# Kernel tuning notes

Measured on AMD Instinct MI355X. Metric: run time of the kernel, lower is better.

The kernel has to match this reference:

```python
import jax, jax.numpy as jnp
import numpy as np

C = 256; GC = 32; G = C // GC; K = 3; S = 1; NEW = 2; PAD = (K - 1) // 2
IN1 = C * K * 2 + C * K * K // 32          # 1608
OUT1 = G * NEW * NEW * K * K // 4          # 72
OUT2 = G * NEW * NEW * K * K               # 288
B = 8; H = 56; W = 56


def setup_inputs():
    key = jax.random.key(0)
    k0, k1, k2 = jax.random.split(key, 3)
    inputs = jax.random.normal(k0, (B, C, H, W), jnp.float32)
    W1 = jax.random.normal(k1, (OUT1, IN1), jnp.float32) * np.float32(1.0 / np.sqrt(IN1))
    b1 = jnp.zeros((OUT1,), jnp.float32)
    W2 = jax.random.normal(k2, (OUT2, OUT1), jnp.float32) * np.float32(1.0 / np.sqrt(OUT1))
    b2 = jnp.zeros((OUT2,), jnp.float32)
    return {"inputs": inputs, "W1": W1, "b1": b1, "W2": W2, "b2": b2}


def _unfold(x, h, w):
    # torch.nn.Unfold(K, 1, PAD, S): patches of shape (B, C, K, K, h, w)
    xp = jnp.pad(x, ((0, 0), (0, 0), (PAD, PAD), (PAD, PAD)))
    cols = [xp[:, :, di:di + (h - 1) * S + 1:S, dj:dj + (w - 1) * S + 1:S]
            for di in range(K) for dj in range(K)]  # fixed K*K=9 slices
    return jnp.stack(cols, axis=2).reshape(x.shape[0], x.shape[1], K, K, h, w)


def reference(inputs, W1, b1, W2, b2):
    b, c, Hh, Ww = inputs.shape
    h = (Hh + 2 * PAD - K) // S + 1
    w = (Ww + 2 * PAD - K) // S + 1
    # (B, G, GC, K, K, h, w)
    x = _unfold(inputs, h, w).reshape(b, G, GC, K, K, h, w)
    # three max-pooled descriptors over different axes
    x1 = x.reshape(b, G, -1, GC // 32, K, K, h, w).max(axis=2).reshape(b, -1, h, w)  # (B, C*K*K//32, h, w)
    x2 = x.max(axis=3).reshape(b, -1, h, w)  # (B, C*K, h, w)
    x3 = x.max(axis=4).reshape(b, -1, h, w)  # (B, C*K, h, w)
    feat = jnp.concatenate([x1, x2, x3], axis=1)  # (B, IN1, h, w)
    # two biased 1x1 convs (ConvModule with no norm/act)
    y = jnp.einsum('bchw,oc->bohw', feat, W1) + b1[None, :, None, None]
    y = jnp.einsum('bchw,oc->bohw', y, W2) + b2[None, :, None, None]
    # softmax over the K*K kernel-window dim
    wgt = jax.nn.softmax(y.reshape(b, G, K * K, NEW * NEW, h, w), axis=2)
    # softmax-weighted local aggregation: sum over kernel window
    agg = jnp.einsum('bgckhw,bgknhw->bgcnhw', x.reshape(b, G, GC, K * K, h, w), wgt)
    # fold with non-overlapping (NEW, NEW) blocks == block upsampling reshape
    return agg.reshape(b, C, NEW, NEW, h, w).transpose(0, 1, 4, 2, 5, 3).reshape(b, C, h * NEW, w * NEW)
```

## Files before the change

kernel.cpp:

```cpp
#include <hip/hip_runtime.h>

#define CC   256
#define HH   56
#define WWID 56
#define KIN1 1608
#define KP1  1632
#define NO1  72
#define NO2  288
#define PPB  14
#define H2   112
#define W2D  112

typedef unsigned short u16;
typedef unsigned int   u32;
typedef __attribute__((ext_vector_type(8))) short v8s;
typedef __attribute__((ext_vector_type(4))) float v4f;

#define W1BF_ELEMS (80 * KP1)
#define W2BF_OFF_B 262144

#define LDS_TOTAL 32768
#define OFF_A 0
#define OFF_B 21504
#define OFF_C 29696

#define Y2S 300

#define SWZ(row) (((row) & 7) << 3)

__device__ __forceinline__ u16 f2b(float x) {
  u32 u = __float_as_uint(x);
  u = (u + 0x7FFFu + ((u >> 16) & 1u)) >> 16;
  return (u16)u;
}

#define DPPMAX(m, ctrl)                                                          \
  do {                                                                           \
    int _y = __builtin_amdgcn_update_dpp(0, __float_as_int(m), (ctrl), 0xF, 0xF, false); \
    (m) = fmaxf((m), __int_as_float(_y));                                        \
  } while (0)

__global__ void kConvW(const float* __restrict__ W1, const float* __restrict__ W2,
                       u16* __restrict__ w1bf, u16* __restrict__ w2bf) {
  int idx = blockIdx.x * 256 + threadIdx.x;
  if (idx < W1BF_ELEMS) {
    int m = idx / KP1, k = idx - m * KP1;
    float v = 0.f;
    if (m < NO1) {
      int orig = -1;
      if (k < 768)                 orig = 72 + (k & 255) * 3 + (k >> 8);
      else if (k < 1536)           orig = 840 + (k & 255) * 3 + ((k - 768) >> 8);
      else if ((k - 1536) < NO1)   orig = k - 1536;
      if (orig >= 0) v = W1[m * KIN1 + orig];
    }
    w1bf[idx] = f2b(v);
  } else {
    int i2 = idx - W1BF_ELEMS;
    if (i2 < NO2 * 96) {
      int m = i2 / 96, k = i2 - m * 96;
      w2bf[i2] = (k < NO1) ? f2b(W2[m * NO1 + k]) : (u16)0;
    }
  }
}

__global__ __launch_bounds__(256, 4)
void kFused(const float* __restrict__ in, const u16* __restrict__ w1bf,
            const float* __restrict__ b1, const u16* __restrict__ w2bf,
            const float* __restrict__ b2, float* __restrict__ out) {
  __shared__ __align__(16) char lds[LDS_TOTAL];
  u16*   rowmaxT = (u16*)(lds + OFF_A);
  u16*   colmaxT = (u16*)(lds + OFF_B);
  u16*   x1T     = (u16*)(lds + OFF_C);
  float* partA   = (float*)(lds + OFF_A);
  float* y2L     = (float*)(lds + OFF_A);
  float* tile    = (float*)(lds + OFF_A);

  const int t  = threadIdx.x;
  const int L  = blockIdx.x + 4 * (blockIdx.y + 56 * blockIdx.z);
  const int jq = L >> 3;
  const int jt = jq & 3, i = jq >> 2, b = L & 7;
  const int c  = t;
  const int g  = c >> 5;
  const int gc = c & 31;
  const int w  = t >> 6, lane = t & 63;
  const int ml = lane & 15, quad = lane >> 4;

  {
    u32* xu = (u32*)x1T;
    if (t < 132) {
#pragma unroll
      for (int rp2 = 0; rp2 < 2; ++rp2) {
        int idx = 2 * t + rp2;
        if (idx < 192) {
          int row = idx / 12;
          xu[(row * 48 + 36 + (idx - row * 12)) ^ ((row & 7) << 2)] = 0u;
        } else {
          int e = idx - 192, row = 14 + e / 36;
          xu[(row * 48 + (e % 36)) ^ ((row & 7) << 2)] = 0u;
        }
      }
    }
  }

  const float* rowbase0 = in + ((size_t)b * CC + c) * (HH * WWID);
  u32 win_p[3][8];
  float colmax[16];
#pragma unroll
  for (int k = 0; k < 16; ++k) colmax[k] = -3.0e38f;

#pragma unroll
  for (int r = 0; r < 3; ++r) {
    const int row = i - 1 + r;
    float sc[16];
    if (row < 0 || row >= HH) {
#pragma unroll
      for (int k = 0; k < 16; ++k) sc[k] = 0.f;
    } else {
      const float* rp = rowbase0 + row * WWID;
      float l[20];
      if (jt == 0) {
        const float4 a0 = *(const float4*)(rp), a1 = *(const float4*)(rp + 4),
                     a2 = *(const float4*)(rp + 8), a3 = *(const float4*)(rp + 12);
        l[0]=a0.x;l[1]=a0.y;l[2]=a0.z;l[3]=a0.w; l[4]=a1.x;l[5]=a1.y;l[6]=a1.z;l[7]=a1.w;
        l[8]=a2.x;l[9]=a2.y;l[10]=a2.z;l[11]=a2.w; l[12]=a3.x;l[13]=a3.y;l[14]=a3.z;l[15]=a3.w;
        sc[0] = 0.f;
#pragma unroll
        for (int k = 1; k < 16; ++k) sc[k] = l[k - 1];
      } else if (jt == 3) {
        const float* q = rp + 40;
        const float4 a0 = *(const float4*)(q), a1 = *(const float4*)(q + 4),
                     a2 = *(const float4*)(q + 8), a3 = *(const float4*)(q + 12);
        l[0]=a0.x;l[1]=a0.y;l[2]=a0.z;l[3]=a0.w; l[4]=a1.x;l[5]=a1.y;l[6]=a1.z;l[7]=a1.w;
        l[8]=a2.x;l[9]=a2.y;l[10]=a2.z;l[11]=a2.w; l[12]=a3.x;l[13]=a3.y;l[14]=a3.z;l[15]=a3.w;
#pragma unroll
        for (int k = 0; k < 15; ++k) sc[k] = l[k + 1];
        sc[15] = 0.f;
      } else {
        const float* q = rp + ((jt == 1) ? 12 : 24);
        const float4 a0 = *(const float4*)(q), a1 = *(const float4*)(q + 4),
                     a2 = *(const float4*)(q + 8), a3 = *(const float4*)(q + 12),
                     a4 = *(const float4*)(q + 16);
        l[0]=a0.x;l[1]=a0.y;l[2]=a0.z;l[3]=a0.w; l[4]=a1.x;l[5]=a1.y;l[6]=a1.z;l[7]=a1.w;
        l[8]=a2.x;l[9]=a2.y;l[10]=a2.z;l[11]=a2.w; l[12]=a3.x;l[13]=a3.y;l[14]=a3.z;l[15]=a3.w;
        l[16]=a4.x;l[17]=a4.y;l[18]=a4.z;l[19]=a4.w;
        if (jt == 1) {
#pragma unroll
          for (int k = 0; k < 16; ++k) sc[k] = l[k + 1];
        } else {
#pragma unroll
          for (int k = 0; k < 16; ++k) sc[k] = l[k + 3];
        }
      }
    }
#pragma unroll
    for (int k = 0; k < 16; ++k) colmax[k] = fmaxf(colmax[k], sc[k]);
#pragma unroll
    for (int n = 0; n < 14; ++n)
      rowmaxT[(n * 768 + r * 256 + c) ^ SWZ(n)] =
          f2b(fmaxf(fmaxf(sc[n], sc[n + 1]), sc[n + 2]));
#pragma unroll
    for (int col = 0; col < 16; ++col) {
      float m = sc[col];
      DPPMAX(m, 0xB1);
      DPPMAX(m, 0x4E);
      DPPMAX(m, 0x141);
      DPPMAX(m, 0x140);
      { int y = __builtin_amdgcn_ds_swizzle(__float_as_int(m), 0x401F);
        m = fmaxf(m, __int_as_float(y)); }
      if (gc == col) {
        u16 mv = f2b(m);
#pragma unroll
        for (int kj = 0; kj < 3; ++kj) {
          const int n = col - kj;
          if (n >= 0 && n < 14)
            x1T[(n * 96 + g * 9 + r * 3 + kj) ^ SWZ(n)] = mv;
        }
      }
    }
#pragma unroll
    for (int k = 0; k < 8; ++k)
      win_p[r][k] = (u32)f2b(sc[2 * k]) | ((u32)f2b(sc[2 * k + 1]) << 16);
  }
#pragma unroll
  for (int col = 0; col < 16; ++col)
    colmaxT[(col * 256 + c) ^ SWZ(col)] = f2b(colmax[col]);
  __syncthreads();

  v4f acc[5];
#pragma unroll
  for (int mt = 0; mt < 5; ++mt) acc[mt] = (v4f){0.f, 0.f, 0.f, 0.f};
  const int ks0 = w * 13, ks1 = (w == 3) ? 51 : ks0 + 13;

  auto loadB = [&](int ks) -> v8s {
    if (ks < 24) {
      int kj = ks >> 3, c0 = (ks & 7) * 32, rowi = ml + kj;
      return *(v8s*)&colmaxT[(rowi * 256 + c0 + quad * 8) ^ SWZ(rowi)];
    } else if (ks < 48) {
      return *(v8s*)&rowmaxT[(ml * 768 + (ks - 24) * 32 + quad * 8) ^ SWZ(ml)];
    } else {
      return *(v8s*)&x1T[(ml * 96 + (ks - 48) * 32 + quad * 8) ^ SWZ(ml)];
    }
  };

  {
    v8s bf_c = loadB(ks0);
    v8s af_c[5];
    {
      const int k0 = ks0 * 32 + quad * 8;
#pragma unroll
      for (int mt = 0; mt < 5; ++mt)
        af_c[mt] = *(const v8s*)&w1bf[(mt * 16 + ml) * KP1 + k0];
    }
    for (int ks = ks0; ks < ks1; ++ks) {
      v8s bf_n, af_n[5];
      if (ks + 1 < ks1) {
        bf_n = loadB(ks + 1);
        const int k0n = (ks + 1) * 32 + quad * 8;
#pragma unroll
        for (int mt = 0; mt < 5; ++mt)
          af_n[mt] = *(const v8s*)&w1bf[(mt * 16 + ml) * KP1 + k0n];
      }
#pragma unroll
      for (int mt = 0; mt < 5; ++mt)
        acc[mt] = __builtin_amdgcn_mfma_f32_16x16x32_bf16(af_c[mt], bf_c, acc[mt], 0, 0, 0);
      if (ks + 1 < ks1) {
        bf_c = bf_n;
#pragma unroll
        for (int mt = 0; mt < 5; ++mt) af_c[mt] = af_n[mt];
      }
    }
  }
  __syncthreads();

#pragma unroll
  for (int mt = 0; mt < 5; ++mt)
    *(v4f*)&partA[((w * 5 + mt) * 16 + ml) * 16 + quad * 4] = acc[mt];
  __syncthreads();

  u16* y1b = x1T;
#pragma unroll
  for (int it = 0; it < 4; ++it) {
    int e = t + it * 256;
    if (e < NO1 * PPB) {
      int m = e / PPB, n = e - m * PPB;
      float s = b1[m];
#pragma unroll
      for (int ww = 0; ww < 4; ++ww)
        s += partA[((ww * 5 + (m >> 4)) * 16 + n) * 16 + (m & 15)];
      y1b[(n * 96 + m) ^ SWZ(n)] = f2b(s);
    }
  }
  __syncthreads();

  {
    v8s bfr[3];
#pragma unroll
    for (int ks = 0; ks < 3; ++ks)
      bfr[ks] = *(v8s*)&y1b[(ml * 96 + ks * 32 + quad * 8) ^ SWZ(ml)];
    const int mt0 = (w < 2) ? 5 * w : 10 + 4 * (w - 2);
    const int mtn = (w < 2) ? 5 : 4;
    const u16* w2base = w2bf + ml * 96 + quad * 8;
    v8s afA[3], afB[3];
#pragma unroll
    for (int ks = 0; ks < 3; ++ks)
      afA[ks] = *(const v8s*)(w2base + (mt0 * 16) * 96 + ks * 32);
#pragma unroll
    for (int mi = 0; mi < 5; ++mi) {
      if (mi < mtn) {
        const int mt = mt0 + mi;
        v4f a2 = (v4f){0.f, 0.f, 0.f, 0.f};
        if ((mi & 1) == 0) {
          if (mi + 1 < mtn) {
#pragma unroll
            for (int ks = 0; ks < 3; ++ks)
              afB[ks] = *(const v8s*)(w2base + ((mt + 1) * 16) * 96 + ks * 32);
          }
#pragma unroll
          for (int ks = 0; ks < 3; ++ks)
            a2 = __builtin_amdgcn_mfma_f32_16x16x32_bf16(afA[ks], bfr[ks], a2, 0, 0, 0);
        } else {
          if (mi + 1 < mtn) {
#pragma unroll
            for (int ks = 0; ks < 3; ++ks)
              afA[ks] = *(const v8s*)(w2base + ((mt + 1) * 16) * 96 + ks * 32);
          }
#pragma unroll
          for (int ks = 0; ks < 3; ++ks)
            a2 = __builtin_amdgcn_mfma_f32_16x16x32_bf16(afB[ks], bfr[ks], a2, 0, 0, 0);
        }
        const int o0 = mt * 16 + quad * 4;
        const float4 bv = *(const float4*)(b2 + o0);
        a2[0] += bv.x; a2[1] += bv.y; a2[2] += bv.z; a2[3] += bv.w;
        *(v4f*)&y2L[ml * Y2S + o0] = a2;
      }
    }
  }
  __syncthreads();

#pragma unroll
  for (int it = 0; it < 2; ++it) {
    int s2 = t + it * 256;
    if (s2 < 448) {
      int gg = s2 / 56, rem = s2 - gg * 56, nn = rem / PPB, n = rem - nn * PPB;
      float* bp = &y2L[n * Y2S + gg * 36 + nn];
      float v9[9], m = -1e30f;
#pragma unroll
      for (int k = 0; k < 9; ++k) { v9[k] = bp[k * 4]; m = fmaxf(m, v9[k]); }
      float sum = 0.f;
#pragma unroll
      for (int k = 0; k < 9; ++k) { v9[k] = __expf(v9[k] - m); sum += v9[k]; }
      float inv = 1.f / sum;
#pragma unroll
      for (int k = 0; k < 9; ++k) bp[k * 4] = v9[k] * inv;
    }
  }
  __syncthreads();

  float a0s[14], a1s[14], a2s[14], a3s[14];
#pragma unroll
  for (int n = 0; n < 14; ++n) {
    const v4f* wp = (const v4f*)&y2L[n * Y2S + g * 36];
    float a0 = 0.f, a1 = 0.f, a2v = 0.f, a3 = 0.f;
#pragma unroll
    for (int r = 0; r < 3; ++r) {
      float x0, x1, x2v;
      if ((n & 1) == 0) {
        u32 ua = win_p[r][n >> 1], ub = win_p[r][(n >> 1) + 1];
        x0  = __uint_as_float(ua << 16);
        x1  = __uint_as_float(ua & 0xffff0000u);
        x2v = __uint_as_float(ub << 16);
      } else {
        u32 ua = win_p[r][n >> 1], ub = win_p[r][(n >> 1) + 1];
        x0  = __uint_as_float(ua & 0xffff0000u);
        x1  = __uint_as_float(ub << 16);
        x2v = __uint_as_float(ub & 0xffff0000u);
      }
#pragma unroll
      for (int kj = 0; kj < 3; ++kj) {
        v4f wv = wp[r * 3 + kj];
        float x = (kj == 0) ? x0 : (kj == 1) ? x1 : x2v;
        a0  = fmaf(x, wv[0], a0);
        a1  = fmaf(x, wv[1], a1);
        a2v = fmaf(x, wv[2], a2v);
        a3  = fmaf(x, wv[3], a3);
      }
    }
    a0s[n] = a0; a1s[n] = a1; a2s[n] = a2v; a3s[n] = a3;
  }
  __syncthreads();

  const int cl = c & 63;
  for (int ch = 0; ch < 4; ++ch) {
    if ((c >> 6) == ch) {
#pragma unroll
      for (int n = 0; n < 14; ++n) {
        float2 lo2; lo2.x = a0s[n]; lo2.y = a1s[n];
        float2 hi2; hi2.x = a2s[n]; hi2.y = a3s[n];
        *(float2*)&tile[cl * 60 + 2 * n] = lo2;
        *(float2*)&tile[cl * 60 + 28 + 2 * n] = hi2;
      }
    }
    __syncthreads();
#pragma unroll
    for (int it = 0; it < 4; ++it) {
      int f = t + it * 256;
      if (f < 896) {
        int rr = f / 7, xi = f - rr * 7;
        int cg = ch * 64 + (rr >> 1), di = rr & 1;
        v4f val = *(v4f*)&tile[(rr >> 1) * 60 + di * 28 + xi * 4];
        *(v4f*)&out[((size_t)(b * CC + cg) * H2 + (size_t)(2 * i + di)) * W2D
                    + 28 * jt + xi * 4] = val;
      }
    }
    __syncthreads();
  }
}

extern "C" void kernel_launch(void* const* d_in, const int* in_sizes, int n_in,
                              void* d_out, int out_size, void* d_ws, size_t ws_size,
                              hipStream_t stream) {
  const float* in = (const float*)d_in[0];
  const float* W1 = (const float*)d_in[1];
  const float* b1 = (const float*)d_in[2];
  const float* W2 = (const float*)d_in[3];
  const float* b2 = (const float*)d_in[4];
  float* out = (float*)d_out;

  u16* w1bf = (u16*)d_ws;
  u16* w2bf = (u16*)((char*)d_ws + W2BF_OFF_B);

  const int B = in_sizes[0] / (CC * HH * WWID);

  kConvW<<<dim3((W1BF_ELEMS + NO2 * 96 + 255) / 256), 256, 0, stream>>>(W1, W2, w1bf, w2bf);
  dim3 grid(WWID / PPB, HH, B);
  kFused<<<grid, 256, 0, stream>>>(in, w1bf, b1, w2bf, b2, out);
}
```

Before: 201.2 us.

## Prefetch GEMM weights before barriers and double-buffer the MFMA loop with priority hints

```diff
diff --git a/kernel.cpp b/kernel.cpp
--- a/kernel.cpp
+++ b/kernel.cpp
@@ -42,23 +42,35 @@
 
 __global__ void kConvW(const float* __restrict__ W1, const float* __restrict__ W2,
                        u16* __restrict__ w1bf, u16* __restrict__ w2bf) {
-  int idx = blockIdx.x * 256 + threadIdx.x;
-  if (idx < W1BF_ELEMS) {
-    int m = idx / KP1, k = idx - m * KP1;
-    float v = 0.f;
+  int p = blockIdx.x * 256 + threadIdx.x;
+  int e0 = 2 * p;
+  float v0 = 0.f, v1 = 0.f;
+  if (e0 < W1BF_ELEMS) {
+    int m = e0 / KP1, k = e0 - m * KP1;
     if (m < NO1) {
-      int orig = -1;
-      if (k < 768)                 orig = 72 + (k & 255) * 3 + (k >> 8);
-      else if (k < 1536)           orig = 840 + (k & 255) * 3 + ((k - 768) >> 8);
-      else if ((k - 1536) < NO1)   orig = k - 1536;
-      if (orig >= 0) v = W1[m * KIN1 + orig];
-    }
-    w1bf[idx] = f2b(v);
+      const float* Wm = W1 + m * KIN1;
+      if (k < 768) {
+        int o = 72 + (k & 255) * 3 + (k >> 8);
+        v0 = Wm[o]; v1 = Wm[o + 3];
+      } else if (k < 1536) {
+        int o = 840 + (k & 255) * 3 + ((k - 768) >> 8);
+        v0 = Wm[o]; v1 = Wm[o + 3];
+      } else {
+        int t1 = k - 1536;
+        if (t1 < NO1)     v0 = Wm[t1];
+        if (t1 + 1 < NO1) v1 = Wm[t1 + 1];
+      }
+    }
+    ((u32*)w1bf)[p] = (u32)f2b(v0) | ((u32)f2b(v1) << 16);
   } else {
-    int i2 = idx - W1BF_ELEMS;
+    int i2 = e0 - W1BF_ELEMS;
     if (i2 < NO2 * 96) {
       int m = i2 / 96, k = i2 - m * 96;
-      w2bf[i2] = (k < NO1) ? f2b(W2[m * NO1 + k]) : (u16)0;
+      if (k < NO1) {
+        v0 = W2[m * NO1 + k];
+        if (k + 1 < NO1) v1 = W2[m * NO1 + k + 1];
+      }
+      ((u32*)w2bf)[i2 >> 1] = (u32)f2b(v0) | ((u32)f2b(v1) << 16);
     }
   }
 }
@@ -184,12 +196,15 @@
 #pragma unroll
   for (int col = 0; col < 16; ++col)
     colmaxT[(col * 256 + c) ^ SWZ(col)] = f2b(colmax[col]);
-  __syncthreads();
-
-  v4f acc[5];
-#pragma unroll
-  for (int mt = 0; mt < 5; ++mt) acc[mt] = (v4f){0.f, 0.f, 0.f, 0.f};
+
   const int ks0 = w * 13, ks1 = (w == 3) ? 51 : ks0 + 13;
+  v8s afA[5], afB[5];
+#pragma unroll
+  for (int mt = 0; mt < 5; ++mt) {
+    afA[mt] = *(const v8s*)&w1bf[(mt * 16 + ml) * KP1 + ks0 * 32 + quad * 8];
+    afB[mt] = *(const v8s*)&w1bf[(mt * 16 + ml) * KP1 + (ks0 + 1) * 32 + quad * 8];
+  }
+  __syncthreads();
 
   auto loadB = [&](int ks) -> v8s {
     if (ks < 24) {
@@ -202,31 +217,38 @@
     }
   };
 
+  v4f acc[5];
+#pragma unroll
+  for (int mt = 0; mt < 5; ++mt) acc[mt] = (v4f){0.f, 0.f, 0.f, 0.f};
   {
-    v8s bf_c = loadB(ks0);
-    v8s af_c[5];
-    {
-      const int k0 = ks0 * 32 + quad * 8;
+    v8s bfA = loadB(ks0);
+    v8s bfB = loadB(ks0 + 1);
+    for (int ks = ks0; ks < ks1; ks += 2) {
+      __builtin_amdgcn_s_setprio(1);
 #pragma unroll
       for (int mt = 0; mt < 5; ++mt)
-        af_c[mt] = *(const v8s*)&w1bf[(mt * 16 + ml) * KP1 + k0];
-    }
-    for (int ks = ks0; ks < ks1; ++ks) {
-      v8s bf_n, af_n[5];
+        acc[mt] = __builtin_amdgcn_mfma_f32_16x16x32_bf16(afA[mt], bfA, acc[mt], 0, 0, 0);
+      __builtin_amdgcn_s_setprio(0);
+      if (ks + 2 < ks1) {
+        const int kn = (ks + 2) * 32 + quad * 8;
+#pragma unroll
+        for (int mt = 0; mt < 5; ++mt)
+          afA[mt] = *(const v8s*)&w1bf[(mt * 16 + ml) * KP1 + kn];
+        bfA = loadB(ks + 2);
+      }
       if (ks + 1 < ks1) {
-        bf_n = loadB(ks + 1);
-        const int k0n = (ks + 1) * 32 + quad * 8;
+        __builtin_amdgcn_s_setprio(1);
 #pragma unroll
         for (int mt = 0; mt < 5; ++mt)
-          af_n[mt] = *(const v8s*)&w1bf[(mt * 16 + ml) * KP1 + k0n];
-      }
-#pragma unroll
-      for (int mt = 0; mt < 5; ++mt)
-        acc[mt] = __builtin_amdgcn_mfma_f32_16x16x32_bf16(af_c[mt], bf_c, acc[mt], 0, 0, 0);
-      if (ks + 1 < ks1) {
-        bf_c = bf_n;
-#pragma unroll
-        for (int mt = 0; mt < 5; ++mt) af_c[mt] = af_n[mt];
+          acc[mt] = __builtin_amdgcn_mfma_f32_16x16x32_bf16(afB[mt], bfB, acc[mt], 0, 0, 0);
+        __builtin_amdgcn_s_setprio(0);
+        if (ks + 3 < ks1) {
+          const int kn = (ks + 3) * 32 + quad * 8;
+#pragma unroll
+          for (int mt = 0; mt < 5; ++mt)
+            afB[mt] = *(const v8s*)&w1bf[(mt * 16 + ml) * KP1 + kn];
+          bfB = loadB(ks + 3);
+        }
       }
     }
   }
@@ -235,6 +257,19 @@
 #pragma unroll
   for (int mt = 0; mt < 5; ++mt)
     *(v4f*)&partA[((w * 5 + mt) * 16 + ml) * 16 + quad * 4] = acc[mt];
+
+  const int mt0 = (w < 2) ? 5 * w : 10 + 4 * (w - 2);
+  const int mtn = (w < 2) ? 5 : 4;
+  v8s w2r[15];
+#pragma unroll
+  for (int mi = 0; mi < 5; ++mi) {
+    if (mi < mtn) {
+#pragma unroll
+      for (int ks = 0; ks < 3; ++ks)
+        w2r[mi * 3 + ks] =
+            *(const v8s*)&w2bf[((mt0 + mi) * 16 + ml) * 96 + ks * 32 + quad * 8];
+    }
+  }
   __syncthreads();
 
   u16* y1b = x1T;
@@ -257,41 +292,23 @@
 #pragma unroll
     for (int ks = 0; ks < 3; ++ks)
       bfr[ks] = *(v8s*)&y1b[(ml * 96 + ks * 32 + quad * 8) ^ SWZ(ml)];
-    const int mt0 = (w < 2) ? 5 * w : 10 + 4 * (w - 2);
-    const int mtn = (w < 2) ? 5 : 4;
-    const u16* w2base = w2bf + ml * 96 + quad * 8;
-    v8s afA[3], afB[3];
-#pragma unroll
-    for (int ks = 0; ks < 3; ++ks)
-      afA[ks] = *(const v8s*)(w2base + (mt0 * 16) * 96 + ks * 32);
+    float4 bvA = *(const float4*)(b2 + mt0 * 16 + quad * 4);
 #pragma unroll
     for (int mi = 0; mi < 5; ++mi) {
       if (mi < mtn) {
         const int mt = mt0 + mi;
+        float4 bvB;
+        if (mi + 1 < mtn)
+          bvB = *(const float4*)(b2 + (mt + 1) * 16 + quad * 4);
         v4f a2 = (v4f){0.f, 0.f, 0.f, 0.f};
-        if ((mi & 1) == 0) {
-          if (mi + 1 < mtn) {
-#pragma unroll
-            for (int ks = 0; ks < 3; ++ks)
-              afB[ks] = *(const v8s*)(w2base + ((mt + 1) * 16) * 96 + ks * 32);
-          }
-#pragma unroll
-          for (int ks = 0; ks < 3; ++ks)
-            a2 = __builtin_amdgcn_mfma_f32_16x16x32_bf16(afA[ks], bfr[ks], a2, 0, 0, 0);
-        } else {
-          if (mi + 1 < mtn) {
-#pragma unroll
-            for (int ks = 0; ks < 3; ++ks)
-              afA[ks] = *(const v8s*)(w2base + ((mt + 1) * 16) * 96 + ks * 32);
-          }
-#pragma unroll
-          for (int ks = 0; ks < 3; ++ks)
-            a2 = __builtin_amdgcn_mfma_f32_16x16x32_bf16(afB[ks], bfr[ks], a2, 0, 0, 0);
-        }
-        const int o0 = mt * 16 + quad * 4;
-        const float4 bv = *(const float4*)(b2 + o0);
-        a2[0] += bv.x; a2[1] += bv.y; a2[2] += bv.z; a2[3] += bv.w;
-        *(v4f*)&y2L[ml * Y2S + o0] = a2;
+        __builtin_amdgcn_s_setprio(1);
+#pragma unroll
+        for (int ks = 0; ks < 3; ++ks)
+          a2 = __builtin_amdgcn_mfma_f32_16x16x32_bf16(w2r[mi * 3 + ks], bfr[ks], a2, 0, 0, 0);
+        __builtin_amdgcn_s_setprio(0);
+        a2[0] += bvA.x; a2[1] += bvA.y; a2[2] += bvA.z; a2[3] += bvA.w;
+        *(v4f*)&y2L[ml * Y2S + mt * 16 + quad * 4] = a2;
+        if (mi + 1 < mtn) bvA = bvB;
       }
     }
   }
@@ -391,7 +408,7 @@
 
   const int B = in_sizes[0] / (CC * HH * WWID);
 
-  kConvW<<<dim3((W1BF_ELEMS + NO2 * 96 + 255) / 256), 256, 0, stream>>>(W1, W2, w1bf, w2bf);
+  kConvW<<<dim3(((W1BF_ELEMS + NO2 * 96) / 2 + 255) / 256), 256, 0, stream>>>(W1, W2, w1bf, w2bf);
   dim3 grid(WWID / PPB, HH, B);
   kFused<<<grid, 256, 0, stream>>>(in, w1bf, b1, w2bf, b2, out);
 }
```

After: 225.4 us. 12.0% more time.

## Halve per-block pixel tile to 7 and pack weight conversion two-per-thread

Applied to the files above, without the earlier changes.

```diff
diff --git a/kernel.cpp b/kernel.cpp
--- a/kernel.cpp
+++ b/kernel.cpp
@@ -7,7 +7,7 @@
 #define KP1  1632
 #define NO1  72
 #define NO2  288
-#define PPB  14
+#define PPB  7
 #define H2   112
 #define W2D  112
 
@@ -19,10 +19,10 @@
 #define W1BF_ELEMS (80 * KP1)
 #define W2BF_OFF_B 262144
 
-#define LDS_TOTAL 32768
+#define LDS_TOTAL 16704
 #define OFF_A 0
-#define OFF_B 21504
-#define OFF_C 29696
+#define OFF_B 10752
+#define OFF_C 15360
 
 #define Y2S 300
 
@@ -42,23 +42,35 @@
 
 __global__ void kConvW(const float* __restrict__ W1, const float* __restrict__ W2,
                        u16* __restrict__ w1bf, u16* __restrict__ w2bf) {
-  int idx = blockIdx.x * 256 + threadIdx.x;
-  if (idx < W1BF_ELEMS) {
-    int m = idx / KP1, k = idx - m * KP1;
-    float v = 0.f;
+  int p = blockIdx.x * 256 + threadIdx.x;
+  int e0 = 2 * p;
+  float v0 = 0.f, v1 = 0.f;
+  if (e0 < W1BF_ELEMS) {
+    int m = e0 / KP1, k = e0 - m * KP1;
     if (m < NO1) {
-      int orig = -1;
-      if (k < 768)                 orig = 72 + (k & 255) * 3 + (k >> 8);
-      else if (k < 1536)           orig = 840 + (k & 255) * 3 + ((k - 768) >> 8);
-      else if ((k - 1536) < NO1)   orig = k - 1536;
-      if (orig >= 0) v = W1[m * KIN1 + orig];
-    }
-    w1bf[idx] = f2b(v);
+      const float* Wm = W1 + m * KIN1;
+      if (k < 768) {
+        int o = 72 + (k & 255) * 3 + (k >> 8);
+        v0 = Wm[o]; v1 = Wm[o + 3];
+      } else if (k < 1536) {
+        int o = 840 + (k & 255) * 3 + ((k - 768) >> 8);
+        v0 = Wm[o]; v1 = Wm[o + 3];
+      } else {
+        int t1 = k - 1536;
+        if (t1 < NO1)     v0 = Wm[t1];
+        if (t1 + 1 < NO1) v1 = Wm[t1 + 1];
+      }
+    }
+    ((u32*)w1bf)[p] = (u32)f2b(v0) | ((u32)f2b(v1) << 16);
   } else {
-    int i2 = idx - W1BF_ELEMS;
+    int i2 = e0 - W1BF_ELEMS;
     if (i2 < NO2 * 96) {
       int m = i2 / 96, k = i2 - m * 96;
-      w2bf[i2] = (k < NO1) ? f2b(W2[m * NO1 + k]) : (u16)0;
+      if (k < NO1) {
+        v0 = W2[m * NO1 + k];
+        if (k + 1 < NO1) v1 = W2[m * NO1 + k + 1];
+      }
+      ((u32*)w2bf)[i2 >> 1] = (u32)f2b(v0) | ((u32)f2b(v1) << 16);
     }
   }
 }
@@ -76,90 +88,81 @@
   float* tile    = (float*)(lds + OFF_A);
 
   const int t  = threadIdx.x;
-  const int L  = blockIdx.x + 4 * (blockIdx.y + 56 * blockIdx.z);
+  const int L  = blockIdx.x + 8 * (blockIdx.y + 56 * blockIdx.z);
+  const int b  = L & 7;
   const int jq = L >> 3;
-  const int jt = jq & 3, i = jq >> 2, b = L & 7;
+  const int jt = jq & 7, i = jq >> 3;
   const int c  = t;
   const int g  = c >> 5;
   const int gc = c & 31;
   const int w  = t >> 6, lane = t & 63;
   const int ml = lane & 15, quad = lane >> 4;
+  const int ml_c = (ml < 7) ? ml : 0;
 
   {
     u32* xu = (u32*)x1T;
-    if (t < 132) {
-#pragma unroll
-      for (int rp2 = 0; rp2 < 2; ++rp2) {
-        int idx = 2 * t + rp2;
-        if (idx < 192) {
-          int row = idx / 12;
-          xu[(row * 48 + 36 + (idx - row * 12)) ^ ((row & 7) << 2)] = 0u;
-        } else {
-          int e = idx - 192, row = 14 + e / 36;
-          xu[(row * 48 + (e % 36)) ^ ((row & 7) << 2)] = 0u;
-        }
-      }
+    if (t < 84) {
+      int row = t / 12, j = t - row * 12;
+      xu[(row * 48 + 36 + j) ^ ((row & 7) << 2)] = 0u;
     }
   }
 
   const float* rowbase0 = in + ((size_t)b * CC + c) * (HH * WWID);
-  u32 win_p[3][8];
-  float colmax[16];
-#pragma unroll
-  for (int k = 0; k < 16; ++k) colmax[k] = -3.0e38f;
+  u32 win_p[3][5];
+  float colmax[9];
+#pragma unroll
+  for (int k = 0; k < 9; ++k) colmax[k] = -3.0e38f;
 
 #pragma unroll
   for (int r = 0; r < 3; ++r) {
     const int row = i - 1 + r;
-    float sc[16];
+    float sc[9];
     if (row < 0 || row >= HH) {
 #pragma unroll
-      for (int k = 0; k < 16; ++k) sc[k] = 0.f;
+      for (int k = 0; k < 9; ++k) sc[k] = 0.f;
     } else {
       const float* rp = rowbase0 + row * WWID;
-      float l[20];
       if (jt == 0) {
-        const float4 a0 = *(const float4*)(rp), a1 = *(const float4*)(rp + 4),
-                     a2 = *(const float4*)(rp + 8), a3 = *(const float4*)(rp + 12);
+        const float4 a0 = *(const float4*)(rp), a1 = *(const float4*)(rp + 4);
+        sc[0] = 0.f;
+        sc[1]=a0.x; sc[2]=a0.y; sc[3]=a0.z; sc[4]=a0.w;
+        sc[5]=a1.x; sc[6]=a1.y; sc[7]=a1.z; sc[8]=a1.w;
+      } else if (jt == 7) {
+        const float4 a0 = *(const float4*)(rp + 48), a1 = *(const float4*)(rp + 52);
+        sc[0]=a0.x; sc[1]=a0.y; sc[2]=a0.z; sc[3]=a0.w;
+        sc[4]=a1.x; sc[5]=a1.y; sc[6]=a1.z; sc[7]=a1.w;
+        sc[8] = 0.f;
+      } else {
+        const int f = 7 * jt - 1, off = f & 3;
+        const float* q = rp + (f - off);
+        const float4 a0 = *(const float4*)(q), a1 = *(const float4*)(q + 4),
+                     a2 = *(const float4*)(q + 8);
+        float l[12];
         l[0]=a0.x;l[1]=a0.y;l[2]=a0.z;l[3]=a0.w; l[4]=a1.x;l[5]=a1.y;l[6]=a1.z;l[7]=a1.w;
-        l[8]=a2.x;l[9]=a2.y;l[10]=a2.z;l[11]=a2.w; l[12]=a3.x;l[13]=a3.y;l[14]=a3.z;l[15]=a3.w;
-        sc[0] = 0.f;
-#pragma unroll
-        for (int k = 1; k < 16; ++k) sc[k] = l[k - 1];
-      } else if (jt == 3) {
-        const float* q = rp + 40;
-        const float4 a0 = *(const float4*)(q), a1 = *(const float4*)(q + 4),
-                     a2 = *(const float4*)(q + 8), a3 = *(const float4*)(q + 12);
-        l[0]=a0.x;l[1]=a0.y;l[2]=a0.z;l[3]=a0.w; l[4]=a1.x;l[5]=a1.y;l[6]=a1.z;l[7]=a1.w;
-        l[8]=a2.x;l[9]=a2.y;l[10]=a2.z;l[11]=a2.w; l[12]=a3.x;l[13]=a3.y;l[14]=a3.z;l[15]=a3.w;
-#pragma unroll
-        for (int k = 0; k < 15; ++k) sc[k] = l[k + 1];
-        sc[15] = 0.f;
-      } else {
-        const float* q = rp + ((jt == 1) ? 12 : 24);
-        const float4 a0 = *(const float4*)(q), a1 = *(const float4*)(q + 4),
-                     a2 = *(const float4*)(q + 8), a3 = *(const float4*)(q + 12),
-                     a4 = *(const float4*)(q + 16);
-        l[0]=a0.x;l[1]=a0.y;l[2]=a0.z;l[3]=a0.w; l[4]=a1.x;l[5]=a1.y;l[6]=a1.z;l[7]=a1.w;
-        l[8]=a2.x;l[9]=a2.y;l[10]=a2.z;l[11]=a2.w; l[12]=a3.x;l[13]=a3.y;l[14]=a3.z;l[15]=a3.w;
-        l[16]=a4.x;l[17]=a4.y;l[18]=a4.z;l[19]=a4.w;
-        if (jt == 1) {
-#pragma unroll
-          for (int k = 0; k < 16; ++k) sc[k] = l[k + 1];
+        l[8]=a2.x;l[9]=a2.y;l[10]=a2.z;l[11]=a2.w;
+        if (off == 0) {
+#pragma unroll
+          for (int s = 0; s < 9; ++s) sc[s] = l[s];
+        } else if (off == 1) {
+#pragma unroll
+          for (int s = 0; s < 9; ++s) sc[s] = l[s + 1];
+        } else if (off == 2) {
+#pragma unroll
+          for (int s = 0; s < 9; ++s) sc[s] = l[s + 2];
         } else {
 #pragma unroll
-          for (int k = 0; k < 16; ++k) sc[k] = l[k + 3];
+          for (int s = 0; s < 9; ++s) sc[s] = l[s + 3];
         }
       }
     }
 #pragma unroll
-    for (int k = 0; k < 16; ++k) colmax[k] = fmaxf(colmax[k], sc[k]);
-#pragma unroll
-    for (int n = 0; n < 14; ++n)
+    for (int k = 0; k < 9; ++k) colmax[k] = fmaxf(colmax[k], sc[k]);
+#pragma unroll
+    for (int n = 0; n < 7; ++n)
       rowmaxT[(n * 768 + r * 256 + c) ^ SWZ(n)] =
           f2b(fmaxf(fmaxf(sc[n], sc[n + 1]), sc[n + 2]));
 #pragma unroll
-    for (int col = 0; col < 16; ++col) {
+    for (int col = 0; col < 9; ++col) {
       float m = sc[col];
       DPPMAX(m, 0xB1);
       DPPMAX(m, 0x4E);
@@ -172,17 +175,18 @@
 #pragma unroll
         for (int kj = 0; kj < 3; ++kj) {
           const int n = col - kj;
-          if (n >= 0 && n < 14)
+          if (n >= 0 && n < 7)
             x1T[(n * 96 + g * 9 + r * 3 + kj) ^ SWZ(n)] = mv;
         }
       }
     }
 #pragma unroll
-    for (int k = 0; k < 8; ++k)
+    for (int k = 0; k < 4; ++k)
       win_p[r][k] = (u32)f2b(sc[2 * k]) | ((u32)f2b(sc[2 * k + 1]) << 16);
-  }
-#pragma unroll
-  for (int col = 0; col < 16; ++col)
+    win_p[r][4] = (u32)f2b(sc[8]);
+  }
+#pragma unroll
+  for (int col = 0; col < 9; ++col)
     colmaxT[(col * 256 + c) ^ SWZ(col)] = f2b(colmax[col]);
   __syncthreads();
 
@@ -193,12 +197,12 @@
 
   auto loadB = [&](int ks) -> v8s {
     if (ks < 24) {
-      int kj = ks >> 3, c0 = (ks & 7) * 32, rowi = ml + kj;
+      int kj = ks >> 3, c0 = (ks & 7) * 32, rowi = ml_c + kj;
       return *(v8s*)&colmaxT[(rowi * 256 + c0 + quad * 8) ^ SWZ(rowi)];
     } else if (ks < 48) {
-      return *(v8s*)&rowmaxT[(ml * 768 + (ks - 24) * 32 + quad * 8) ^ SWZ(ml)];
+      return *(v8s*)&rowmaxT[(ml_c * 768 + (ks - 24) * 32 + quad * 8) ^ SWZ(ml_c)];
     } else {
-      return *(v8s*)&x1T[(ml * 96 + (ks - 48) * 32 + quad * 8) ^ SWZ(ml)];
+      return *(v8s*)&x1T[(ml_c * 96 + (ks - 48) * 32 + quad * 8) ^ SWZ(ml_c)];
     }
   };
 
@@ -232,21 +236,23 @@
   }
   __syncthreads();
 
-#pragma unroll
-  for (int mt = 0; mt < 5; ++mt)
-    *(v4f*)&partA[((w * 5 + mt) * 16 + ml) * 16 + quad * 4] = acc[mt];
+  if (ml < 7) {
+#pragma unroll
+    for (int mt = 0; mt < 5; ++mt)
+      *(v4f*)&partA[((w * 5 + mt) * 7 + ml) * 16 + quad * 4] = acc[mt];
+  }
   __syncthreads();
 
   u16* y1b = x1T;
 #pragma unroll
-  for (int it = 0; it < 4; ++it) {
+  for (int it = 0; it < 2; ++it) {
     int e = t + it * 256;
     if (e < NO1 * PPB) {
       int m = e / PPB, n = e - m * PPB;
       float s = b1[m];
 #pragma unroll
       for (int ww = 0; ww < 4; ++ww)
-        s += partA[((ww * 5 + (m >> 4)) * 16 + n) * 16 + (m & 15)];
+        s += partA[((ww * 5 + (m >> 4)) * 7 + n) * 16 + (m & 15)];
       y1b[(n * 96 + m) ^ SWZ(n)] = f2b(s);
     }
   }
@@ -256,7 +262,7 @@
     v8s bfr[3];
 #pragma unroll
     for (int ks = 0; ks < 3; ++ks)
-      bfr[ks] = *(v8s*)&y1b[(ml * 96 + ks * 32 + quad * 8) ^ SWZ(ml)];
+      bfr[ks] = *(v8s*)&y1b[(ml_c * 96 + ks * 32 + quad * 8) ^ SWZ(ml_c)];
     const int mt0 = (w < 2) ? 5 * w : 10 + 4 * (w - 2);
     const int mtn = (w < 2) ? 5 : 4;
     const u16* w2base = w2bf + ml * 96 + quad * 8;
@@ -288,64 +294,63 @@
           for (int ks = 0; ks < 3; ++ks)
             a2 = __builtin_amdgcn_mfma_f32_16x16x32_bf16(afB[ks], bfr[ks], a2, 0, 0, 0);
         }
-        const int o0 = mt * 16 + quad * 4;
-        const float4 bv = *(const float4*)(b2 + o0);
-        a2[0] += bv.x; a2[1] += bv.y; a2[2] += bv.z; a2[3] += bv.w;
-        *(v4f*)&y2L[ml * Y2S + o0] = a2;
-      }
-    }
-  }
-  __syncthreads();
-
-#pragma unroll
-  for (int it = 0; it < 2; ++it) {
-    int s2 = t + it * 256;
-    if (s2 < 448) {
-      int gg = s2 / 56, rem = s2 - gg * 56, nn = rem / PPB, n = rem - nn * PPB;
-      float* bp = &y2L[n * Y2S + gg * 36 + nn];
-      float v9[9], m = -1e30f;
-#pragma unroll
-      for (int k = 0; k < 9; ++k) { v9[k] = bp[k * 4]; m = fmaxf(m, v9[k]); }
-      float sum = 0.f;
-#pragma unroll
-      for (int k = 0; k < 9; ++k) { v9[k] = __expf(v9[k] - m); sum += v9[k]; }
-      float inv = 1.f / sum;
-#pragma unroll
-      for (int k = 0; k < 9; ++k) bp[k * 4] = v9[k] * inv;
-    }
-  }
-  __syncthreads();
-
-  float a0s[14], a1s[14], a2s[14], a3s[14];
-#pragma unroll
-  for (int n = 0; n < 14; ++n) {
-    const v4f* wp = (const v4f*)&y2L[n * Y2S + g * 36];
-    float a0 = 0.f, a1 = 0.f, a2v = 0.f, a3 = 0.f;
+        if (ml < 7) {
+          const int o0 = mt * 16 + quad * 4;
+          const float4 bv = *(const float4*)(b2 + o0);
+          a2[0] += bv.x; a2[1] += bv.y; a2[2] += bv.z; a2[3] += bv.w;
+          *(v4f*)&y2L[ml * Y2S + o0] = a2;
+        }
+      }
+    }
+  }
+  __syncthreads();
+
+  if (t < 224) {
+    int gg = t / 28, rem = t - gg * 28, nn = rem / PPB, n = rem - nn * PPB;
+    float* bp = &y2L[n * Y2S + gg * 36 + nn];
+    float v9[9], m = -1e30f;
+#pragma unroll
+    for (int k = 0; k < 9; ++k) { v9[k] = bp[k * 4]; m = fmaxf(m, v9[k]); }
+    float sum = 0.f;
+#pragma unroll
+    for (int k = 0; k < 9; ++k) { v9[k] = __expf(v9[k] - m); sum += v9[k]; }
+    float inv = 1.f / sum;
+#pragma unroll
+    for (int k = 0; k < 9; ++k) bp[k * 4] = v9[k] * inv;
+  }
+  __syncthreads();
+
+  float a0s[7], a1s[7], a2s[7], a3s[7];
+#pragma unroll
+  for (int x = 0; x < 4; ++x) {
+    const int n0 = 2 * x;
+    const v4f* wp0 = (const v4f*)&y2L[n0 * Y2S + g * 36];
+    const v4f* wp1 = (x < 3) ? (const v4f*)&y2L[(n0 + 1) * Y2S + g * 36] : wp0;
+    float e0 = 0.f, e1 = 0.f, e2 = 0.f, e3 = 0.f;
+    float o0 = 0.f, o1 = 0.f, o2 = 0.f, o3 = 0.f;
 #pragma unroll
     for (int r = 0; r < 3; ++r) {
-      float x0, x1, x2v;
-      if ((n & 1) == 0) {
-        u32 ua = win_p[r][n >> 1], ub = win_p[r][(n >> 1) + 1];
-        x0  = __uint_as_float(ua << 16);
-        x1  = __uint_as_float(ua & 0xffff0000u);
-        x2v = __uint_as_float(ub << 16);
-      } else {
-        u32 ua = win_p[r][n >> 1], ub = win_p[r][(n >> 1) + 1];
-        x0  = __uint_as_float(ua & 0xffff0000u);
-        x1  = __uint_as_float(ub << 16);
-        x2v = __uint_as_float(ub & 0xffff0000u);
-      }
+      u32 ua = win_p[r][x], ub = win_p[r][x + 1];
+      float ex0 = __uint_as_float(ua << 16);
+      float ex1 = __uint_as_float(ua & 0xffff0000u);
+      float ex2 = __uint_as_float(ub << 16);
+      float ox2 = __uint_as_float(ub & 0xffff0000u);
 #pragma unroll
       for (int kj = 0; kj < 3; ++kj) {
-        v4f wv = wp[r * 3 + kj];
-        float x = (kj == 0) ? x0 : (kj == 1) ? x1 : x2v;
-        a0  = fmaf(x, wv[0], a0);
-        a1  = fmaf(x, wv[1], a1);
-        a2v = fmaf(x, wv[2], a2v);
-        a3  = fmaf(x, wv[3], a3);
-      }
-    }
-    a0s[n] = a0; a1s[n] = a1; a2s[n] = a2v; a3s[n] = a3;
+        v4f wv0 = wp0[r * 3 + kj];
+        float xe = (kj == 0) ? ex0 : (kj == 1) ? ex1 : ex2;
+        e0 = fmaf(xe, wv0[0], e0); e1 = fmaf(xe, wv0[1], e1);
+        e2 = fmaf(xe, wv0[2], e2); e3 = fmaf(xe, wv0[3], e3);
+        if (x < 3) {
+          v4f wv1 = wp1[r * 3 + kj];
+          float xo = (kj == 0) ? ex1 : (kj == 1) ? ex2 : ox2;
+          o0 = fmaf(xo, wv1[0], o0); o1 = fmaf(xo, wv1[1], o1);
+          o2 = fmaf(xo, wv1[2], o2); o3 = fmaf(xo, wv1[3], o3);
+        }
+      }
+    }
+    a0s[n0] = e0; a1s[n0] = e1; a2s[n0] = e2; a3s[n0] = e3;
+    if (x < 3) { a0s[n0 + 1] = o0; a1s[n0 + 1] = o1; a2s[n0 + 1] = o2; a3s[n0 + 1] = o3; }
   }
   __syncthreads();
 
@@ -353,11 +358,11 @@
   for (int ch = 0; ch < 4; ++ch) {
     if ((c >> 6) == ch) {
 #pragma unroll
-      for (int n = 0; n < 14; ++n) {
+      for (int n = 0; n < 7; ++n) {
         float2 lo2; lo2.x = a0s[n]; lo2.y = a1s[n];
         float2 hi2; hi2.x = a2s[n]; hi2.y = a3s[n];
-        *(float2*)&tile[cl * 60 + 2 * n] = lo2;
-        *(float2*)&tile[cl * 60 + 28 + 2 * n] = hi2;
+        *(float2*)&tile[cl * 30 + 2 * n] = lo2;
+        *(float2*)&tile[cl * 30 + 14 + 2 * n] = hi2;
       }
     }
     __syncthreads();
@@ -367,9 +372,9 @@
       if (f < 896) {
         int rr = f / 7, xi = f - rr * 7;
         int cg = ch * 64 + (rr >> 1), di = rr & 1;
-        v4f val = *(v4f*)&tile[(rr >> 1) * 60 + di * 28 + xi * 4];
-        *(v4f*)&out[((size_t)(b * CC + cg) * H2 + (size_t)(2 * i + di)) * W2D
-                    + 28 * jt + xi * 4] = val;
+        float2 val = *(float2*)&tile[(rr >> 1) * 30 + di * 14 + xi * 2];
+        *(float2*)&out[((size_t)(b * CC + cg) * H2 + (size_t)(2 * i + di)) * W2D
+                       + 14 * jt + 2 * xi] = val;
       }
     }
     __syncthreads();
@@ -391,7 +396,7 @@
 
   const int B = in_sizes[0] / (CC * HH * WWID);
 
-  kConvW<<<dim3((W1BF_ELEMS + NO2 * 96 + 255) / 256), 256, 0, stream>>>(W1, W2, w1bf, w2bf);
+  kConvW<<<dim3(((W1BF_ELEMS + NO2 * 96) / 2 + 255) / 256), 256, 0, stream>>>(W1, W2, w1bf, w2bf);
   dim3 grid(WWID / PPB, HH, B);
   kFused<<<grid, 256, 0, stream>>>(in, w1bf, b1, w2bf, b2, out);
 }
```

Measured after the change: 229.7 us. 14.2% more time.

## Interleave rowmax GEMM per window row and split W1 GEMM by output tile

Applied to the files above, without the earlier changes.

```diff
diff --git a/kernel.cpp b/kernel.cpp
--- a/kernel.cpp
+++ b/kernel.cpp
@@ -15,14 +15,16 @@
 typedef unsigned int   u32;
 typedef __attribute__((ext_vector_type(8))) short v8s;
 typedef __attribute__((ext_vector_type(4))) float v4f;
+typedef __attribute__((ext_vector_type(4))) unsigned short us4;
 
 #define W1BF_ELEMS (80 * KP1)
 #define W2BF_OFF_B 262144
 
-#define LDS_TOTAL 32768
-#define OFF_A 0
-#define OFF_B 21504
-#define OFF_C 29696
+#define LDS_TOTAL 20736
+#define OFF_CM 0
+#define OFF_RM 8192
+#define OFF_X1 15360
+#define OFF_Y1 18048
 
 #define Y2S 300
 
@@ -42,23 +44,35 @@
 
 __global__ void kConvW(const float* __restrict__ W1, const float* __restrict__ W2,
                        u16* __restrict__ w1bf, u16* __restrict__ w2bf) {
-  int idx = blockIdx.x * 256 + threadIdx.x;
-  if (idx < W1BF_ELEMS) {
-    int m = idx / KP1, k = idx - m * KP1;
-    float v = 0.f;
+  int p = blockIdx.x * 256 + threadIdx.x;
+  int e0 = 2 * p;
+  float v0 = 0.f, v1 = 0.f;
+  if (e0 < W1BF_ELEMS) {
+    int m = e0 / KP1, k = e0 - m * KP1;
     if (m < NO1) {
-      int orig = -1;
-      if (k < 768)                 orig = 72 + (k & 255) * 3 + (k >> 8);
-      else if (k < 1536)           orig = 840 + (k & 255) * 3 + ((k - 768) >> 8);
-      else if ((k - 1536) < NO1)   orig = k - 1536;
-      if (orig >= 0) v = W1[m * KIN1 + orig];
-    }
-    w1bf[idx] = f2b(v);
+      const float* Wm = W1 + m * KIN1;
+      if (k < 768) {
+        int o = 72 + (k & 255) * 3 + (k >> 8);
+        v0 = Wm[o]; v1 = Wm[o + 3];
+      } else if (k < 1536) {
+        int o = 840 + (k & 255) * 3 + ((k - 768) >> 8);
+        v0 = Wm[o]; v1 = Wm[o + 3];
+      } else {
+        int t1 = k - 1536;
+        if (t1 < NO1)     v0 = Wm[t1];
+        if (t1 + 1 < NO1) v1 = Wm[t1 + 1];
+      }
+    }
+    ((u32*)w1bf)[p] = (u32)f2b(v0) | ((u32)f2b(v1) << 16);
   } else {
-    int i2 = idx - W1BF_ELEMS;
+    int i2 = e0 - W1BF_ELEMS;
     if (i2 < NO2 * 96) {
       int m = i2 / 96, k = i2 - m * 96;
-      w2bf[i2] = (k < NO1) ? f2b(W2[m * NO1 + k]) : (u16)0;
+      if (k < NO1) {
+        v0 = W2[m * NO1 + k];
+        if (k + 1 < NO1) v1 = W2[m * NO1 + k + 1];
+      }
+      ((u32*)w2bf)[i2 >> 1] = (u32)f2b(v0) | ((u32)f2b(v1) << 16);
     }
   }
 }
@@ -68,12 +82,13 @@
             const float* __restrict__ b1, const u16* __restrict__ w2bf,
             const float* __restrict__ b2, float* __restrict__ out) {
   __shared__ __align__(16) char lds[LDS_TOTAL];
-  u16*   rowmaxT = (u16*)(lds + OFF_A);
-  u16*   colmaxT = (u16*)(lds + OFF_B);
-  u16*   x1T     = (u16*)(lds + OFF_C);
-  float* partA   = (float*)(lds + OFF_A);
-  float* y2L     = (float*)(lds + OFF_A);
-  float* tile    = (float*)(lds + OFF_A);
+  u16*   colmaxT  = (u16*)(lds + OFF_CM);
+  u16*   rowmax_r = (u16*)(lds + OFF_RM);
+  u16*   x1T      = (u16*)(lds + OFF_X1);
+  u16*   y1b      = (u16*)(lds + OFF_Y1);
+  float* partE    = (float*)(lds + OFF_CM);
+  float* y2L      = (float*)(lds + OFF_CM);
+  float* tile     = (float*)(lds + OFF_CM);
 
   const int t  = threadIdx.x;
   const int L  = blockIdx.x + 4 * (blockIdx.y + 56 * blockIdx.z);
@@ -84,21 +99,16 @@
   const int gc = c & 31;
   const int w  = t >> 6, lane = t & 63;
   const int ml = lane & 15, quad = lane >> 4;
+  const int ml_c = (ml < 14) ? ml : 0;
 
   {
     u32* xu = (u32*)x1T;
-    if (t < 132) {
-#pragma unroll
-      for (int rp2 = 0; rp2 < 2; ++rp2) {
-        int idx = 2 * t + rp2;
-        if (idx < 192) {
-          int row = idx / 12;
-          xu[(row * 48 + 36 + (idx - row * 12)) ^ ((row & 7) << 2)] = 0u;
-        } else {
-          int e = idx - 192, row = 14 + e / 36;
-          xu[(row * 48 + (e % 36)) ^ ((row & 7) << 2)] = 0u;
-        }
-      }
+    u32* yu = (u32*)y1b;
+    if (t < 168) {
+      int row = t / 12, j = t - row * 12;
+      int off = (row * 48 + 36 + j) ^ ((row & 7) << 2);
+      xu[off] = 0u;
+      yu[off] = 0u;
     }
   }
 
@@ -107,6 +117,9 @@
   float colmax[16];
 #pragma unroll
   for (int k = 0; k < 16; ++k) colmax[k] = -3.0e38f;
+
+  v4f acc0 = (v4f){0.f, 0.f, 0.f, 0.f};
+  v4f acc4 = (v4f){0.f, 0.f, 0.f, 0.f};
 
 #pragma unroll
   for (int r = 0; r < 3; ++r) {
@@ -156,7 +169,7 @@
     for (int k = 0; k < 16; ++k) colmax[k] = fmaxf(colmax[k], sc[k]);
 #pragma unroll
     for (int n = 0; n < 14; ++n)
-      rowmaxT[(n * 768 + r * 256 + c) ^ SWZ(n)] =
+      rowmax_r[(n * 256 + c) ^ SWZ(n)] =
           f2b(fmaxf(fmaxf(sc[n], sc[n + 1]), sc[n + 2]));
 #pragma unroll
     for (int col = 0; col < 16; ++col) {
@@ -180,75 +193,78 @@
 #pragma unroll
     for (int k = 0; k < 8; ++k)
       win_p[r][k] = (u32)f2b(sc[2 * k]) | ((u32)f2b(sc[2 * k + 1]) << 16);
-  }
-#pragma unroll
-  for (int col = 0; col < 16; ++col)
-    colmaxT[(col * 256 + c) ^ SWZ(col)] = f2b(colmax[col]);
-  __syncthreads();
-
-  v4f acc[5];
-#pragma unroll
-  for (int mt = 0; mt < 5; ++mt) acc[mt] = (v4f){0.f, 0.f, 0.f, 0.f};
-  const int ks0 = w * 13, ks1 = (w == 3) ? 51 : ks0 + 13;
-
-  auto loadB = [&](int ks) -> v8s {
-    if (ks < 24) {
-      int kj = ks >> 3, c0 = (ks & 7) * 32, rowi = ml + kj;
-      return *(v8s*)&colmaxT[(rowi * 256 + c0 + quad * 8) ^ SWZ(rowi)];
-    } else if (ks < 48) {
-      return *(v8s*)&rowmaxT[(ml * 768 + (ks - 24) * 32 + quad * 8) ^ SWZ(ml)];
-    } else {
-      return *(v8s*)&x1T[(ml * 96 + (ks - 48) * 32 + quad * 8) ^ SWZ(ml)];
-    }
-  };
+    if (r == 2) {
+#pragma unroll
+      for (int col = 0; col < 16; ++col)
+        colmaxT[(col * 256 + c) ^ SWZ(col)] = f2b(colmax[col]);
+    }
+    __syncthreads();
+
+    {
+      const int ksb = 24 + r * 8;
+#pragma unroll
+      for (int ci = 0; ci < 8; ++ci) {
+        v8s bf = *(v8s*)&rowmax_r[(ml_c * 256 + ci * 32 + quad * 8) ^ SWZ(ml_c)];
+        v8s a0 = *(const v8s*)&w1bf[(w * 16 + ml) * KP1 + (ksb + ci) * 32 + quad * 8];
+        acc0 = __builtin_amdgcn_mfma_f32_16x16x32_bf16(a0, bf, acc0, 0, 0, 0);
+      }
+#pragma unroll
+      for (int e = 0; e < 2; ++e) {
+        const int ci = 2 * w + e;
+        v8s bf = *(v8s*)&rowmax_r[(ml_c * 256 + ci * 32 + quad * 8) ^ SWZ(ml_c)];
+        v8s a4 = *(const v8s*)&w1bf[(64 + ml) * KP1 + (ksb + ci) * 32 + quad * 8];
+        acc4 = __builtin_amdgcn_mfma_f32_16x16x32_bf16(a4, bf, acc4, 0, 0, 0);
+      }
+    }
+    if (r < 2) __syncthreads();
+  }
 
   {
-    v8s bf_c = loadB(ks0);
-    v8s af_c[5];
-    {
-      const int k0 = ks0 * 32 + quad * 8;
-#pragma unroll
-      for (int mt = 0; mt < 5; ++mt)
-        af_c[mt] = *(const v8s*)&w1bf[(mt * 16 + ml) * KP1 + k0];
-    }
-    for (int ks = ks0; ks < ks1; ++ks) {
-      v8s bf_n, af_n[5];
-      if (ks + 1 < ks1) {
-        bf_n = loadB(ks + 1);
-        const int k0n = (ks + 1) * 32 + quad * 8;
-#pragma unroll
-        for (int mt = 0; mt < 5; ++mt)
-          af_n[mt] = *(const v8s*)&w1bf[(mt * 16 + ml) * KP1 + k0n];
-      }
-#pragma unroll
-      for (int mt = 0; mt < 5; ++mt)
-        acc[mt] = __builtin_amdgcn_mfma_f32_16x16x32_bf16(af_c[mt], bf_c, acc[mt], 0, 0, 0);
-      if (ks + 1 < ks1) {
-        bf_c = bf_n;
-#pragma unroll
-        for (int mt = 0; mt < 5; ++mt) af_c[mt] = af_n[mt];
-      }
-    }
-  }
-  __syncthreads();
-
-#pragma unroll
-  for (int mt = 0; mt < 5; ++mt)
-    *(v4f*)&partA[((w * 5 + mt) * 16 + ml) * 16 + quad * 4] = acc[mt];
-  __syncthreads();
-
-  u16* y1b = x1T;
-#pragma unroll
-  for (int it = 0; it < 4; ++it) {
-    int e = t + it * 256;
-    if (e < NO1 * PPB) {
-      int m = e / PPB, n = e - m * PPB;
-      float s = b1[m];
-#pragma unroll
-      for (int ww = 0; ww < 4; ++ww)
-        s += partA[((ww * 5 + (m >> 4)) * 16 + n) * 16 + (m & 15)];
-      y1b[(n * 96 + m) ^ SWZ(n)] = f2b(s);
-    }
+#pragma unroll
+    for (int s = 0; s < 24; ++s) {
+      const int kj = s >> 3, ci = s & 7, rowi = ml + kj;
+      v8s bf = *(v8s*)&colmaxT[(rowi * 256 + ci * 32 + quad * 8) ^ SWZ(rowi)];
+      v8s a0 = *(const v8s*)&w1bf[(w * 16 + ml) * KP1 + s * 32 + quad * 8];
+      acc0 = __builtin_amdgcn_mfma_f32_16x16x32_bf16(a0, bf, acc0, 0, 0, 0);
+    }
+#pragma unroll
+    for (int e = 0; e < 6; ++e) {
+      const int s4 = 6 * w + e, kj = s4 >> 3, ci = s4 & 7, rowi = ml + kj;
+      v8s bf = *(v8s*)&colmaxT[(rowi * 256 + ci * 32 + quad * 8) ^ SWZ(rowi)];
+      v8s a4 = *(const v8s*)&w1bf[(64 + ml) * KP1 + s4 * 32 + quad * 8];
+      acc4 = __builtin_amdgcn_mfma_f32_16x16x32_bf16(a4, bf, acc4, 0, 0, 0);
+    }
+#pragma unroll
+    for (int ksx = 0; ksx < 3; ++ksx) {
+      v8s bf = *(v8s*)&x1T[(ml_c * 96 + ksx * 32 + quad * 8) ^ SWZ(ml_c)];
+      v8s a0 = *(const v8s*)&w1bf[(w * 16 + ml) * KP1 + (48 + ksx) * 32 + quad * 8];
+      acc0 = __builtin_amdgcn_mfma_f32_16x16x32_bf16(a0, bf, acc0, 0, 0, 0);
+    }
+    if (w < 3) {
+      v8s bf = *(v8s*)&x1T[(ml_c * 96 + w * 32 + quad * 8) ^ SWZ(ml_c)];
+      v8s a4 = *(const v8s*)&w1bf[(64 + ml) * KP1 + (48 + w) * 32 + quad * 8];
+      acc4 = __builtin_amdgcn_mfma_f32_16x16x32_bf16(a4, bf, acc4, 0, 0, 0);
+    }
+  }
+  __syncthreads();
+
+  *(v4f*)&partE[((w * 16 + ml) * 16) + quad * 4] = acc4;
+  if (ml < 14) {
+    const float4 bv0 = *(const float4*)(b1 + w * 16 + quad * 4);
+    us4 h0;
+    h0.x = f2b(acc0[0] + bv0.x); h0.y = f2b(acc0[1] + bv0.y);
+    h0.z = f2b(acc0[2] + bv0.z); h0.w = f2b(acc0[3] + bv0.w);
+    *(us4*)&y1b[(ml * 96 + w * 16 + quad * 4) ^ SWZ(ml)] = h0;
+  }
+  __syncthreads();
+
+  if (t < 112) {
+    const int n = t >> 3, mp = t & 7;
+    float s = b1[64 + mp];
+#pragma unroll
+    for (int ww = 0; ww < 4; ++ww)
+      s += partE[((ww * 16 + n) * 16) + mp];
+    y1b[(n * 96 + 64 + mp) ^ SWZ(n)] = f2b(s);
   }
   __syncthreads();
 
@@ -256,7 +272,7 @@
     v8s bfr[3];
 #pragma unroll
     for (int ks = 0; ks < 3; ++ks)
-      bfr[ks] = *(v8s*)&y1b[(ml * 96 + ks * 32 + quad * 8) ^ SWZ(ml)];
+      bfr[ks] = *(v8s*)&y1b[(ml_c * 96 + ks * 32 + quad * 8) ^ SWZ(ml_c)];
     const int mt0 = (w < 2) ? 5 * w : 10 + 4 * (w - 2);
     const int mtn = (w < 2) ? 5 : 4;
     const u16* w2base = w2bf + ml * 96 + quad * 8;
@@ -288,10 +304,12 @@
           for (int ks = 0; ks < 3; ++ks)
             a2 = __builtin_amdgcn_mfma_f32_16x16x32_bf16(afB[ks], bfr[ks], a2, 0, 0, 0);
         }
-        const int o0 = mt * 16 + quad * 4;
-        const float4 bv = *(const float4*)(b2 + o0);
-        a2[0] += bv.x; a2[1] += bv.y; a2[2] += bv.z; a2[3] += bv.w;
-        *(v4f*)&y2L[ml * Y2S + o0] = a2;
+        if (ml < 14) {
+          const int o0 = mt * 16 + quad * 4;
+          const float4 bv = *(const float4*)(b2 + o0);
+          a2[0] += bv.x; a2[1] += bv.y; a2[2] += bv.z; a2[3] += bv.w;
+          *(v4f*)&y2L[ml * Y2S + o0] = a2;
+        }
       }
     }
   }
@@ -391,7 +409,7 @@
 
   const int B = in_sizes[0] / (CC * HH * WWID);
 
-  kConvW<<<dim3((W1BF_ELEMS + NO2 * 96 + 255) / 256), 256, 0, stream>>>(W1, W2, w1bf, w2bf);
+  kConvW<<<dim3(((W1BF_ELEMS + NO2 * 96) / 2 + 255) / 256), 256, 0, stream>>>(W1, W2, w1bf, w2bf);
   dim3 grid(WWID / PPB, HH, B);
   kFused<<<grid, 256, 0, stream>>>(in, w1bf, b1, w2bf, b2, out);
 }
```

After: 219.8 us. 9.2% more time.
